# Kernel optimization log

Measured on AMD Instinct MI355X. Metric: run time of the kernel, lower is better.

The kernel has to match this reference:

```python
import jax, jax.numpy as jnp
import numpy as np

TAU = 2.0       # LIF tau for both spiking and non-spiking nodes
T = 16          # number of SNN timesteps
EPS = 1e-5      # BatchNorm eps
V_TH = 1.0      # LIF threshold (spikingjelly default)

B, P, F_IN, H, A = 64, 16, 672, 2048, 32


def _bn(x, g, b, m, v):
    # BatchNorm1d over channel axis P (axis -2 of [..., P, F]), eval mode
    inv = jax.lax.rsqrt(v + EPS)
    return (x - m[:, None]) * (inv * g)[:, None] + b[:, None]


def _spike(x):
    # heaviside(x) as in spikingjelly (x >= 0 -> 1)
    return (x >= 0.0).astype(x.dtype)


def setup_inputs() -> dict:
    key = jax.random.key(0)
    ks = jax.random.split(key, 8)
    d = {
        "x": jax.random.normal(ks[0], (B, P, F_IN), jnp.float32),
        "w1": jax.random.normal(ks[1], (F_IN, H), jnp.float32) * (1.0 / np.sqrt(F_IN)),
        "bias1": jax.random.normal(ks[2], (H,), jnp.float32) * 0.01,
        "w2": jax.random.normal(ks[3], (H, A), jnp.float32) * (1.0 / np.sqrt(H)),
        "bias2": jax.random.normal(ks[4], (A,), jnp.float32) * 0.01,
    }
    kk = jax.random.split(ks[5], 12)
    for i, pre in enumerate(["bn0", "bn1", "bn2"]):
        d[pre + "_g"] = jax.random.uniform(kk[4 * i + 0], (P,), jnp.float32, 0.5, 1.5)
        d[pre + "_b"] = jax.random.normal(kk[4 * i + 1], (P,), jnp.float32) * 0.1
        d[pre + "_m"] = jax.random.normal(kk[4 * i + 2], (P,), jnp.float32) * 0.1
        d[pre + "_v"] = jax.random.uniform(kk[4 * i + 3], (P,), jnp.float32, 0.5, 1.5)
    return d


def _forward(x, w1, bias1, w2, bias2,
             bn0_g, bn0_b, bn0_m, bn0_v,
             bn1_g, bn1_b, bn1_m, bn1_v,
             bn2_g, bn2_b, bn2_m, bn2_v):
    # self.norm on the (reshaped) xlstm output: [B, P, 672]
    x = _bn(x, bn0_g, bn0_b, bn0_m, bn0_v)
    # Multi-step mode repeats the same input each timestep, so the
    # timestep-independent Linear+BN is hoisted out of the T loop.
    h = jnp.einsum("bpf,fh->bph", x, w1) + bias1          # [B, P, H]
    h = _bn(h, bn1_g, bn1_b, bn1_m, bn1_v)

    # LIF neuron: decay_input=True, v_reset=0, hard reset, threshold 1
    def lif_step(v, _):
        v = v + (h - v) / TAU
        s = _spike(v - V_TH)
        v = v * (1.0 - s)  # hard reset to v_reset=0
        return v, s

    _, spikes = jax.lax.scan(lif_step, jnp.zeros_like(h), None, length=T)  # [T,B,P,H]

    y = jnp.einsum("tbph,ha->tbpa", spikes, w2) + bias2    # [T, B, P, A]
    y = _bn(y, bn2_g, bn2_b, bn2_m, bn2_v)

    # NonSpikingLIF: charge only, output v each step
    def ns_step(v, yt):
        v = v + (yt - v) / TAU
        return v, v

    _, vs = jax.lax.scan(ns_step, jnp.zeros(y.shape[1:], y.dtype), y)  # [T,B,P,A]
    return jnp.tanh(vs.mean(0)) * 2.0                      # action [B, P, A]


def reference(x, w1, bias1, w2, bias2,
              bn0_g, bn0_b, bn0_m, bn0_v,
              bn1_g, bn1_b, bn1_m, bn1_v,
              bn2_g, bn2_b, bn2_m, bn2_v):
    return _forward(x, w1, bias1, w2, bias2,
                    bn0_g, bn0_b, bn0_m, bn0_v,
                    bn1_g, bn1_b, bn1_m, bn1_v,
                    bn2_g, bn2_b, bn2_m, bn2_v)
```

## Files before the change

kernel.cpp:

```cpp
#include <hip/hip_runtime.h>
#include <math.h>

#define BB 64
#define PP 16
#define FIN 672
#define HH 2048
#define AA 32
#define MM (BB*PP)
#define EPSBN 1e-5f
#define NKB 21

typedef _Float16 f16;
typedef __attribute__((ext_vector_type(8))) _Float16 half8;
typedef __attribute__((ext_vector_type(4))) float floatx4;

__device__ const float LIF_LUT[18] = {
    0.0f,
    0.93750095367431640625f,
    0.4583339691162109375f,
    0.294643402099609375f,
    0.21666717529296875f,
    0.1713714599609375f,
    0.123016357421875f,
    0.11712646484375f,
    0.0936279296875f,
    0.062255859375f,
    0.06201171875f,
    0.0615234375f,
    0.060546875f,
    0.05859375f,
    0.0546875f,
    0.046875f,
    0.03125f,
    0.0f
};

__global__ __launch_bounds__(256) void k_prep(
    const float* __restrict__ x, const float* __restrict__ w1,
    const float* __restrict__ w2,
    const float* __restrict__ g0, const float* __restrict__ b0,
    const float* __restrict__ m0, const float* __restrict__ v0,
    f16* __restrict__ Ah, f16* __restrict__ Al,
    f16* __restrict__ Wh, f16* __restrict__ Wl,
    f16* __restrict__ W2h, f16* __restrict__ W2l)
{
    __shared__ float sbuf[32 * 65];
    const int tid = threadIdx.x;
    const int b   = blockIdx.x;

    if (b < 448) {
        const int mb = b / 7;
        const int kc = b % 7;
        #pragma unroll
        for (int i = 0; i < 2; ++i) {
            const int f4 = tid + 256 * i;
            if (f4 < 384) {
                const int row = f4 / 24;
                const int c4  = (f4 % 24) * 4;
                float4 v = *(const float4*)(x + (size_t)(mb * 16 + row) * FIN + kc * 96 + c4);
                sbuf[row * 97 + c4 + 0] = v.x; sbuf[row * 97 + c4 + 1] = v.y;
                sbuf[row * 97 + c4 + 2] = v.z; sbuf[row * 97 + c4 + 3] = v.w;
            }
        }
        __syncthreads();
        if (tid < 192) {
            const int fi   = tid >> 6;
            const int lane = tid & 63;
            const int row  = lane & 15;
            const int koff = fi * 32 + ((lane >> 4) << 3);
            const float a0  = g0[row] / sqrtf(v0[row] + EPSBN);
            const float be0 = b0[row] - m0[row] * a0;
            half8 hi, lo;
            #pragma unroll
            for (int j = 0; j < 8; ++j) {
                const float xn = fmaf(a0, sbuf[row * 97 + koff + j], be0);
                const f16 h = (f16)xn;
                hi[j] = h;
                lo[j] = (f16)(xn - (float)h);
            }
            const int kb = kc * 3 + fi;
            const size_t idx = ((size_t)(mb * NKB + kb) * 64 + lane);
            *(half8*)(Ah + idx * 8) = hi;
            *(half8*)(Al + idx * 8) = lo;
        }
    } else if (b < 1120) {
        const int bw = b - 448;
        const int ng = bw & 31;
        const int kb = bw >> 5;
        #pragma unroll
        for (int i = 0; i < 2; ++i) {
            const int f4  = tid + 256 * i;
            const int row = f4 >> 4;
            const int c4  = (f4 & 15) * 4;
            float4 v = *(const float4*)(w1 + (size_t)(kb * 32 + row) * HH + ng * 64 + c4);
            sbuf[row * 65 + c4 + 0] = v.x; sbuf[row * 65 + c4 + 1] = v.y;
            sbuf[row * 65 + c4 + 2] = v.z; sbuf[row * 65 + c4 + 3] = v.w;
        }
        __syncthreads();
        const int fi   = tid >> 6;
        const int lane = tid & 63;
        const int col  = fi * 16 + (lane & 15);
        const int kr   = (lane >> 4) << 3;
        half8 hi, lo;
        #pragma unroll
        for (int j = 0; j < 8; ++j) {
            const float wv = sbuf[(kr + j) * 65 + col];
            const f16 h = (f16)wv;
            hi[j] = h;
            lo[j] = (f16)(wv - (float)h);
        }
        const int nb = ng * 4 + fi;
        const size_t idx = ((size_t)(nb * NKB + kb) * 64 + lane);
        *(half8*)(Wh + idx * 8) = hi;
        *(half8*)(Wl + idx * 8) = lo;
    } else {
        const int kb2 = b - 1120;
        const int row = tid >> 3;
        const int c4  = (tid & 7) << 2;
        float4 v = *(const float4*)(w2 + (size_t)(kb2 * 32 + row) * AA + c4);
        sbuf[row * 33 + c4 + 0] = v.x; sbuf[row * 33 + c4 + 1] = v.y;
        sbuf[row * 33 + c4 + 2] = v.z; sbuf[row * 33 + c4 + 3] = v.w;
        __syncthreads();
        if (tid < 128) {
            const int nb   = tid >> 6;
            const int lane = tid & 63;
            const int col  = nb * 16 + (lane & 15);
            const int kr   = (lane >> 4) << 3;
            half8 hi, lo;
            #pragma unroll
            for (int j = 0; j < 8; ++j) {
                const float wv = sbuf[(kr + j) * 33 + col];
                const f16 h = (f16)wv;
                hi[j] = h;
                lo[j] = (f16)(wv - (float)h);
            }
            const size_t idx = ((size_t)(kb2 * 2 + nb) * 64 + lane);
            *(half8*)(W2h + idx * 8) = hi;
            *(half8*)(W2l + idx * 8) = lo;
        }
    }
}

#define GLOAD16(g, l) __builtin_amdgcn_global_load_lds(                        \
    (const __attribute__((address_space(1))) void*)(g),                       \
    (__attribute__((address_space(3))) void*)(l), 16, 0, 0)

__global__ __launch_bounds__(256) void k_gemm12(
    const f16* __restrict__ Ah, const f16* __restrict__ Al,
    const f16* __restrict__ Wh, const f16* __restrict__ Wl,
    const f16* __restrict__ W2h, const f16* __restrict__ W2l,
    const float* __restrict__ bias1,
    const float* __restrict__ g1, const float* __restrict__ b1,
    const float* __restrict__ m1, const float* __restrict__ v1,
    float* __restrict__ part)
{
    __shared__ __align__(16) char smem[2 * 16 * 1024];

    const int tid  = threadIdx.x;
    const int lane = tid & 63;
    const int w    = tid >> 6;
    const int wm   = w >> 1, wn = w & 1;

    const int b   = blockIdx.x;
    const int xcd = b & 7;
    const int idx = b >> 3;
    const int bm  = (xcd >> 2) * 8 + (idx >> 3);
    const int bn  = (xcd & 3) * 8 + (idx & 7);
    const int mb0 = bm * 4;
    const int nb0 = bn * 4;

    const char* src[4];
    int ldsoff[4];
    #pragma unroll
    for (int q = 0; q < 4; ++q) {
        const int c = w * 4 + q;
        const char* plane; int tile;
        if (c < 4)       { plane = (const char*)Ah; tile = mb0 + c; }
        else if (c < 8)  { plane = (const char*)Al; tile = mb0 + (c - 4); }
        else if (c < 12) { plane = (const char*)Wh; tile = nb0 + (c - 8); }
        else             { plane = (const char*)Wl; tile = nb0 + (c - 12); }
        src[q]    = plane + (size_t)tile * (NKB * 1024) + lane * 16;
        ldsoff[q] = c * 1024;
    }

#define STAGE(kb, bufsel) do {                                                \
    _Pragma("unroll") for (int q_ = 0; q_ < 4; ++q_)                          \
        GLOAD16(src[q_] + (kb) * 1024, smem + (bufsel) * 16384 + ldsoff[q_]); \
} while (0)

    floatx4 acc00 = (floatx4){0.f,0.f,0.f,0.f};
    floatx4 acc01 = (floatx4){0.f,0.f,0.f,0.f};
    floatx4 acc10 = (floatx4){0.f,0.f,0.f,0.f};
    floatx4 acc11 = (floatx4){0.f,0.f,0.f,0.f};

    STAGE(0, 0);
    __syncthreads();

    int cur = 0;
    for (int kb = 0; kb < NKB; ++kb) {
        if (kb + 1 < NKB) STAGE(kb + 1, cur ^ 1);

        const char* base = smem + cur * 16384 + lane * 16;
        half8 ah0 = *(const half8*)(base + (wm * 2 + 0) * 1024);
        half8 ah1 = *(const half8*)(base + (wm * 2 + 1) * 1024);
        half8 al0 = *(const half8*)(base + (4 + wm * 2 + 0) * 1024);
        half8 al1 = *(const half8*)(base + (4 + wm * 2 + 1) * 1024);
        half8 wh0 = *(const half8*)(base + (8 + wn * 2 + 0) * 1024);
        half8 wh1 = *(const half8*)(base + (8 + wn * 2 + 1) * 1024);
        half8 wl0 = *(const half8*)(base + (12 + wn * 2 + 0) * 1024);
        half8 wl1 = *(const half8*)(base + (12 + wn * 2 + 1) * 1024);

        acc00 = __builtin_amdgcn_mfma_f32_16x16x32_f16(ah0, wh0, acc00, 0,0,0);
        acc01 = __builtin_amdgcn_mfma_f32_16x16x32_f16(ah0, wh1, acc01, 0,0,0);
        acc10 = __builtin_amdgcn_mfma_f32_16x16x32_f16(ah1, wh0, acc10, 0,0,0);
        acc11 = __builtin_amdgcn_mfma_f32_16x16x32_f16(ah1, wh1, acc11, 0,0,0);
        acc00 = __builtin_amdgcn_mfma_f32_16x16x32_f16(ah0, wl0, acc00, 0,0,0);
        acc01 = __builtin_amdgcn_mfma_f32_16x16x32_f16(ah0, wl1, acc01, 0,0,0);
        acc10 = __builtin_amdgcn_mfma_f32_16x16x32_f16(ah1, wl0, acc10, 0,0,0);
        acc11 = __builtin_amdgcn_mfma_f32_16x16x32_f16(ah1, wl1, acc11, 0,0,0);
        acc00 = __builtin_amdgcn_mfma_f32_16x16x32_f16(al0, wh0, acc00, 0,0,0);
        acc01 = __builtin_amdgcn_mfma_f32_16x16x32_f16(al0, wh1, acc01, 0,0,0);
        acc10 = __builtin_amdgcn_mfma_f32_16x16x32_f16(al1, wh0, acc10, 0,0,0);
        acc11 = __builtin_amdgcn_mfma_f32_16x16x32_f16(al1, wh1, acc11, 0,0,0);

        __syncthreads();
        cur ^= 1;
    }
#undef STAGE

    f16* Sl = (f16*)smem;
    const float H16 = (float)(65536.0 / 65535.0);
    const int   r4  = (lane >> 4) << 2;
    float a1c[4], be1c[4];
    #pragma unroll
    for (int j = 0; j < 4; ++j) {
        const int p = r4 + j;
        a1c[j]  = g1[p] / sqrtf(v1[p] + EPSBN);
        be1c[j] = b1[p] - m1[p] * a1c[j];
    }

    const floatx4 accs[4] = {acc00, acc01, acc10, acc11};
    #pragma unroll
    for (int m = 0; m < 2; ++m) {
        const int rloc = (wm * 2 + m) * 16 + r4;
        #pragma unroll
        for (int n = 0; n < 2; ++n) {
            const int cloc = (wn * 2 + n) * 16 + (lane & 15);
            const float bs = bias1[nb0 * 16 + cloc];
            const floatx4 a4 = accs[m * 2 + n];
            #pragma unroll
            for (int j = 0; j < 4; ++j) {
                const float h = fmaf(a1c[j], a4[j] + bs, be1c[j]);
                float s = 0.f;
                if (h >= H16) {
                    const float rr = 1.f - __builtin_amdgcn_rcpf(h);
                    int mi = (int)ceilf(-__log2f(rr));
                    mi = mi < 1 ? 1 : (mi > 17 ? 17 : mi);
                    s = LIF_LUT[mi];
                }
                Sl[(rloc + j) * 72 + cloc] = (f16)s;
            }
        }
    }
    __syncthreads();

    floatx4 y0 = (floatx4){0.f,0.f,0.f,0.f};
    floatx4 y1 = (floatx4){0.f,0.f,0.f,0.f};
    const int rsl = (w * 16 + (lane & 15)) * 72 + ((lane >> 4) << 3);
    #pragma unroll
    for (int kb = 0; kb < 2; ++kb) {
        half8 sa = *(const half8*)(Sl + rsl + kb * 32);
        const int hb = bn * 2 + kb;
        half8 wh0 = *(const half8*)(W2h + ((size_t)(hb * 2 + 0) * 64 + lane) * 8);
        half8 wh1 = *(const half8*)(W2h + ((size_t)(hb * 2 + 1) * 64 + lane) * 8);
        half8 wl0 = *(const half8*)(W2l + ((size_t)(hb * 2 + 0) * 64 + lane) * 8);
        half8 wl1 = *(const half8*)(W2l + ((size_t)(hb * 2 + 1) * 64 + lane) * 8);
        y0 = __builtin_amdgcn_mfma_f32_16x16x32_f16(sa, wh0, y0, 0,0,0);
        y0 = __builtin_amdgcn_mfma_f32_16x16x32_f16(sa, wl0, y0, 0,0,0);
        y1 = __builtin_amdgcn_mfma_f32_16x16x32_f16(sa, wh1, y1, 0,0,0);
        y1 = __builtin_amdgcn_mfma_f32_16x16x32_f16(sa, wl1, y1, 0,0,0);
    }
    const int prow = bm * 64 + w * 16 + r4;
    float* pp = part + (size_t)bn * (MM * AA) + (size_t)prow * AA + (lane & 15);
    #pragma unroll
    for (int j = 0; j < 4; ++j) {
        pp[j * AA]      = y0[j];
        pp[j * AA + 16] = y1[j];
    }
}

__global__ __launch_bounds__(256) void k_finish32(
    const float* __restrict__ part, const float* __restrict__ bias2,
    const float* __restrict__ g2, const float* __restrict__ b2,
    const float* __restrict__ m2, const float* __restrict__ v2,
    float* __restrict__ out)
{
    const int i   = blockIdx.x * 256 + threadIdx.x;
    const int col = i & 31;
    const int row = i >> 5;
    const int p   = row & 15;
    float acc = 0.f;
    #pragma unroll
    for (int s = 0; s < 32; ++s) acc += part[(size_t)s * MM * AA + i];
    const float a2   = g2[p] / sqrtf(v2[p] + EPSBN);
    const float be2  = b2[p] - m2[p] * a2;
    const float Csum = 0.9375f + 0x1p-20f;
    const float val  = fmaf(a2, acc + Csum * bias2[col], Csum * be2);
    out[i] = 2.0f * tanhf(val);
}

__global__ __launch_bounds__(256) void k_gemm1_fp32(
    const float* __restrict__ x, const float* __restrict__ w1,
    const float* __restrict__ bias1,
    const float* __restrict__ g0, const float* __restrict__ b0,
    const float* __restrict__ m0, const float* __restrict__ v0,
    const float* __restrict__ g1, const float* __restrict__ b1,
    const float* __restrict__ m1, const float* __restrict__ v1,
    f16* __restrict__ S)
{
    __shared__ float As[16][36];
    __shared__ float Bs[16][68];

    const int tid = threadIdx.x;
    const int bx  = blockIdx.x;
    const int by  = blockIdx.y;

    const int ar   = tid & 31;
    const int ak   = (tid >> 5) << 1;
    const int grow = by * 32 + ar;
    const int pA   = grow & 15;
    const float a0  = g0[pA] / sqrtf(v0[pA] + EPSBN);
    const float be0 = b0[pA] - m0[pA] * a0;
    const float* xrow = x + (size_t)grow * FIN;

    const int brk = tid >> 4;
    const int bcc = (tid & 15) << 2;
    const float* wp = w1 + (size_t)brk * HH + bx * 64 + bcc;

    const int tx = tid & 15;
    const int ty = tid >> 4;

    float acc[2][4];
    #pragma unroll
    for (int i = 0; i < 2; ++i)
        #pragma unroll
        for (int j = 0; j < 4; ++j) acc[i][j] = 0.f;

    float2 aPre = *(const float2*)(xrow + ak);
    float4 bPre = *(const float4*)(wp);

    for (int kt = 0; kt < FIN; kt += 16) {
        As[ak + 0][ar] = fmaf(a0, aPre.x, be0);
        As[ak + 1][ar] = fmaf(a0, aPre.y, be0);
        *(float4*)&Bs[brk][bcc] = bPre;
        __syncthreads();
        if (kt + 16 < FIN) {
            aPre = *(const float2*)(xrow + kt + 16 + ak);
            bPre = *(const float4*)(wp + (size_t)(kt + 16) * HH);
        }
        #pragma unroll
        for (int k = 0; k < 16; ++k) {
            float2 a2 = *(const float2*)&As[k][ty << 1];
            float4 b4 = *(const float4*)&Bs[k][tx << 2];
            float aa[2] = {a2.x, a2.y};
            float bb[4] = {b4.x, b4.y, b4.z, b4.w};
            #pragma unroll
            for (int i = 0; i < 2; ++i)
                #pragma unroll
                for (int j = 0; j < 4; ++j)
                    acc[i][j] = fmaf(aa[i], bb[j], acc[i][j]);
        }
        __syncthreads();
    }

    const float KC[16] = {
        (1.0f-0x1p-16f)*0.0625f,(1.0f-0x1p-15f)*0.0625f,(1.0f-0x1p-14f)*0.0625f,(1.0f-0x1p-13f)*0.0625f,
        (1.0f-0x1p-12f)*0.0625f,(1.0f-0x1p-11f)*0.0625f,(1.0f-0x1p-10f)*0.0625f,(1.0f-0x1p-9f)*0.0625f,
        (1.0f-0x1p-8f)*0.0625f,(1.0f-0x1p-7f)*0.0625f,(1.0f-0x1p-6f)*0.0625f,(1.0f-0x1p-5f)*0.0625f,
        (1.0f-0x1p-4f)*0.0625f,(1.0f-0x1p-3f)*0.0625f,(1.0f-0x1p-2f)*0.0625f,(1.0f-0x1p-1f)*0.0625f
    };

    const int col0 = bx * 64 + (tx << 2);
    float4 bias4 = *(const float4*)(bias1 + col0);
    const float bias_arr[4] = {bias4.x, bias4.y, bias4.z, bias4.w};

    #pragma unroll
    for (int i = 0; i < 2; ++i) {
        const int r = by * 32 + (ty << 1) + i;
        const int p = r & 15;
        const float a1  = g1[p] / sqrtf(v1[p] + EPSBN);
        const float be1 = b1[p] - m1[p] * a1;
        #pragma unroll
        for (int j = 0; j < 4; ++j) {
            const float h = fmaf(a1, acc[i][j] + bias_arr[j], be1);
            float v = 0.f, s = 0.f;
            #pragma unroll
            for (int t = 0; t < 16; ++t) {
                v = v + (h - v) * 0.5f;
                if (v >= 1.0f) { s += KC[t]; v = 0.f; }
            }
            S[(size_t)r * HH + col0 + j] = (f16)s;
        }
    }
}

__global__ __launch_bounds__(256) void k_gemm2_part(
    const f16* __restrict__ S, const float* __restrict__ w2,
    float* __restrict__ part2)
{
    __shared__ float w2s[8192];
    const int tid = threadIdx.x;
    const int rg  = blockIdx.x;
    const int kc  = blockIdx.y;

    const float4* src = (const float4*)(w2 + (size_t)kc * 8192);
    #pragma unroll
    for (int i = tid; i < 2048; i += 256) ((float4*)w2s)[i] = src[i];
    __syncthreads();

    const int rw  = tid >> 5;
    const int col = tid & 31;
    const int row = rg * 8 + rw;
    const f16* Sp = S + (size_t)row * HH + kc * 256;

    float acc0 = 0.f, acc1 = 0.f;
    #pragma unroll 4
    for (int j = 0; j < 256; j += 8) {
        half8 s8 = *(const half8*)(Sp + j);
        acc0 = fmaf((float)s8[0], w2s[(j + 0) * 32 + col], acc0);
        acc1 = fmaf((float)s8[1], w2s[(j + 1) * 32 + col], acc1);
        acc0 = fmaf((float)s8[2], w2s[(j + 2) * 32 + col], acc0);
        acc1 = fmaf((float)s8[3], w2s[(j + 3) * 32 + col], acc1);
        acc0 = fmaf((float)s8[4], w2s[(j + 4) * 32 + col], acc0);
        acc1 = fmaf((float)s8[5], w2s[(j + 5) * 32 + col], acc1);
        acc0 = fmaf((float)s8[6], w2s[(j + 6) * 32 + col], acc0);
        acc1 = fmaf((float)s8[7], w2s[(j + 7) * 32 + col], acc1);
    }
    part2[((size_t)kc * MM + row) * AA + col] = acc0 + acc1;
}

__global__ __launch_bounds__(256) void k_finish8(
    const float* __restrict__ part2, const float* __restrict__ bias2,
    const float* __restrict__ g2, const float* __restrict__ b2,
    const float* __restrict__ m2, const float* __restrict__ v2,
    float* __restrict__ out)
{
    const int i   = blockIdx.x * 256 + threadIdx.x;
    const int col = i & 31;
    const int row = i >> 5;
    const int p   = row & 15;
    float acc = 0.f;
    #pragma unroll
    for (int s = 0; s < 8; ++s) acc += part2[(size_t)s * MM * AA + i];
    const float a2   = g2[p] / sqrtf(v2[p] + EPSBN);
    const float be2  = b2[p] - m2[p] * a2;
    const float Csum = 0.9375f + 0x1p-20f;
    const float val  = fmaf(a2, acc + Csum * bias2[col], Csum * be2);
    out[i] = 2.0f * tanhf(val);
}

extern "C" void kernel_launch(void* const* d_in, const int* in_sizes, int n_in,
                              void* d_out, int out_size, void* d_ws, size_t ws_size,
                              hipStream_t stream) {
    (void)in_sizes; (void)n_in; (void)out_size;
    const float* x     = (const float*)d_in[0];
    const float* w1    = (const float*)d_in[1];
    const float* bias1 = (const float*)d_in[2];
    const float* w2    = (const float*)d_in[3];
    const float* bias2 = (const float*)d_in[4];
    const float* g0 = (const float*)d_in[5];
    const float* b0 = (const float*)d_in[6];
    const float* m0 = (const float*)d_in[7];
    const float* v0 = (const float*)d_in[8];
    const float* g1 = (const float*)d_in[9];
    const float* b1 = (const float*)d_in[10];
    const float* m1 = (const float*)d_in[11];
    const float* v1 = (const float*)d_in[12];
    const float* g2 = (const float*)d_in[13];
    const float* b2 = (const float*)d_in[14];
    const float* m2 = (const float*)d_in[15];
    const float* v2 = (const float*)d_in[16];
    float* out = (float*)d_out;

    const size_t offAl  = 1376256;
    const size_t offWh  = 2752512;
    const size_t offWl  = 5505024;
    const size_t offW2h = 8257536;
    const size_t offW2l = 8388608;
    const size_t offP   = 8519680;
    const size_t needed = offP + 4194304;

    if (ws_size >= needed) {
        f16* Ah  = (f16*)d_ws;
        f16* Al  = (f16*)((char*)d_ws + offAl);
        f16* Wh  = (f16*)((char*)d_ws + offWh);
        f16* Wl  = (f16*)((char*)d_ws + offWl);
        f16* W2h = (f16*)((char*)d_ws + offW2h);
        f16* W2l = (f16*)((char*)d_ws + offW2l);
        float* part = (float*)((char*)d_ws + offP);

        k_prep<<<1184, 256, 0, stream>>>(x, w1, w2, g0, b0, m0, v0,
                                         Ah, Al, Wh, Wl, W2h, W2l);
        k_gemm12<<<512, 256, 0, stream>>>(Ah, Al, Wh, Wl, W2h, W2l, bias1,
                                          g1, b1, m1, v1, part);
        k_finish32<<<128, 256, 0, stream>>>(part, bias2, g2, b2, m2, v2, out);
    } else {
        f16* S       = (f16*)d_ws;
        float* part2 = (float*)((char*)d_ws + (size_t)MM * HH * sizeof(f16));
        k_gemm1_fp32<<<dim3(32, 32), 256, 0, stream>>>(x, w1, bias1,
                                                       g0, b0, m0, v0,
                                                       g1, b1, m1, v1, S);
        k_gemm2_part<<<dim3(128, 8), 256, 0, stream>>>(S, w2, part2);
        k_finish8<<<128, 256, 0, stream>>>(part2, bias2, g2, b2, m2, v2, out);
    }
}
```

Measured before the change: 31.27 us.

## Fuse final split-N reduction into GEMM kernel via last-block atomic counter

Removes the separate finish kernel by having each GEMM block bump a per-row-block atomic counter after writing its partials; the last of the 32 column blocks for a row block reduces the partials and applies BN2, bias and tanh. Counters are zeroed by an extra block appended to the prep kernel. This saves one kernel launch and its gap, but serialises the reduction onto 16 tail blocks, which may lengthen the critical path.

```diff
diff --git a/kernel.cpp b/kernel.cpp
--- a/kernel.cpp
+++ b/kernel.cpp
@@ -42,11 +42,17 @@
     const float* __restrict__ m0, const float* __restrict__ v0,
     f16* __restrict__ Ah, f16* __restrict__ Al,
     f16* __restrict__ Wh, f16* __restrict__ Wl,
-    f16* __restrict__ W2h, f16* __restrict__ W2l)
+    f16* __restrict__ W2h, f16* __restrict__ W2l,
+    int* __restrict__ cnt)
 {
     __shared__ float sbuf[32 * 65];
     const int tid = threadIdx.x;
     const int b   = blockIdx.x;
+
+    if (b >= 1184) {
+        if (tid < 16) cnt[tid] = 0;
+        return;
+    }
 
     if (b < 448) {
         const int mb = b / 7;
@@ -152,9 +158,14 @@
     const float* __restrict__ bias1,
     const float* __restrict__ g1, const float* __restrict__ b1,
     const float* __restrict__ m1, const float* __restrict__ v1,
-    float* __restrict__ part)
+    const float* __restrict__ bias2,
+    const float* __restrict__ g2, const float* __restrict__ b2,
+    const float* __restrict__ m2, const float* __restrict__ v2,
+    float* __restrict__ part, int* __restrict__ cnt,
+    float* __restrict__ out)
 {
     __shared__ __align__(16) char smem[2 * 16 * 1024];
+    __shared__ int isLast;
 
     const int tid  = threadIdx.x;
     const int lane = tid & 63;
@@ -287,26 +298,31 @@
         pp[j * AA]      = y0[j];
         pp[j * AA + 16] = y1[j];
     }
-}
-
-__global__ __launch_bounds__(256) void k_finish32(
-    const float* __restrict__ part, const float* __restrict__ bias2,
-    const float* __restrict__ g2, const float* __restrict__ b2,
-    const float* __restrict__ m2, const float* __restrict__ v2,
-    float* __restrict__ out)
-{
-    const int i   = blockIdx.x * 256 + threadIdx.x;
-    const int col = i & 31;
-    const int row = i >> 5;
-    const int p   = row & 15;
-    float acc = 0.f;
-    #pragma unroll
-    for (int s = 0; s < 32; ++s) acc += part[(size_t)s * MM * AA + i];
-    const float a2   = g2[p] / sqrtf(v2[p] + EPSBN);
-    const float be2  = b2[p] - m2[p] * a2;
-    const float Csum = 0.9375f + 0x1p-20f;
-    const float val  = fmaf(a2, acc + Csum * bias2[col], Csum * be2);
-    out[i] = 2.0f * tanhf(val);
+
+    __threadfence();
+    __syncthreads();
+    if (tid == 0) {
+        const int old = atomicAdd(&cnt[bm], 1);
+        isLast = (old == 31) ? 1 : 0;
+    }
+    __syncthreads();
+    if (isLast) {
+        __threadfence();
+        const float Csum = 0.9375f + 0x1p-20f;
+        for (int o = tid; o < 64 * AA; o += 256) {
+            const int i   = bm * (64 * AA) + o;
+            const int col = i & 31;
+            const int row = i >> 5;
+            const int p   = row & 15;
+            float acc = 0.f;
+            #pragma unroll
+            for (int s = 0; s < 32; ++s) acc += part[(size_t)s * MM * AA + i];
+            const float a2v = g2[p] / sqrtf(v2[p] + EPSBN);
+            const float be2 = b2[p] - m2[p] * a2v;
+            const float val = fmaf(a2v, acc + Csum * bias2[col], Csum * be2);
+            out[i] = 2.0f * tanhf(val);
+        }
+    }
 }
 
 __global__ __launch_bounds__(256) void k_gemm1_fp32(
@@ -488,7 +504,8 @@
     const size_t offW2h = 8257536;
     const size_t offW2l = 8388608;
     const size_t offP   = 8519680;
-    const size_t needed = offP + 4194304;
+    const size_t offCnt = offP + 4194304;
+    const size_t needed = offCnt + 64;
 
     if (ws_size >= needed) {
         f16* Ah  = (f16*)d_ws;
@@ -498,12 +515,14 @@
         f16* W2h = (f16*)((char*)d_ws + offW2h);
         f16* W2l = (f16*)((char*)d_ws + offW2l);
         float* part = (float*)((char*)d_ws + offP);
-
-        k_prep<<<1184, 256, 0, stream>>>(x, w1, w2, g0, b0, m0, v0,
-                                         Ah, Al, Wh, Wl, W2h, W2l);
+        int*   cnt  = (int*)((char*)d_ws + offCnt);
+
+        k_prep<<<1185, 256, 0, stream>>>(x, w1, w2, g0, b0, m0, v0,
+                                         Ah, Al, Wh, Wl, W2h, W2l, cnt);
         k_gemm12<<<512, 256, 0, stream>>>(Ah, Al, Wh, Wl, W2h, W2l, bias1,
-                                          g1, b1, m1, v1, part);
-        k_finish32<<<128, 256, 0, stream>>>(part, bias2, g2, b2, m2, v2, out);
+                                          g1, b1, m1, v1,
+                                          bias2, g2, b2, m2, v2,
+                                          part, cnt, out);
     } else {
         f16* S       = (f16*)d_ws;
         float* part2 = (float*)((char*)d_ws + (size_t)MM * HH * sizeof(f16));
```

After: 97.83 us. +212.9%, slower.
